# Kernel tuning notes

Measured on AMD Instinct MI355X. Metric: run time of the kernel, lower is better.

Reference implementation:

```python
import jax, jax.numpy as jnp
import numpy as np

RES = (256, 256, 256)

# 8 cube corners for trilinear splat/interp
_CORNERS = jnp.array([[i, j, k] for i in (0, 1) for j in (0, 1) for k in (0, 1)], dtype=jnp.int32)


def _corner_idx_weights(pts):
    # pts: (B,P,3) in [0,1). Returns periodic corner indices (B,P,8,3) and trilinear weights (B,P,8).
    resf = jnp.array(RES, dtype=pts.dtype)
    x = pts * resf
    ind0 = jnp.floor(x)
    frac = x - ind0  # (B,P,3)
    idx = (ind0.astype(jnp.int32)[:, :, None, :] + _CORNERS) % jnp.array(RES, dtype=jnp.int32)
    w = jnp.prod(jnp.where(_CORNERS == 1, frac[:, :, None, :], 1.0 - frac[:, :, None, :]), axis=-1)
    return idx, w


def point_rasterize(pts, vals):
    # Periodic trilinear scatter of vals (B,P,F) at pts (B,P,3) into grid (B,r0,r1,r2,F).
    B, P, _ = pts.shape
    F = vals.shape[-1]
    idx, w = _corner_idx_weights(pts)
    flat = (idx[..., 0] * RES[1] + idx[..., 1]) * RES[2] + idx[..., 2]  # (B,P,8)
    contrib = vals[:, :, None, :] * w[..., None]  # (B,P,8,F)
    Rtot = RES[0] * RES[1] * RES[2]
    grid = jax.vmap(lambda s, c: jax.ops.segment_sum(c, s, num_segments=Rtot))(
        flat.reshape(B, -1), contrib.reshape(B, -1, F))
    return grid.reshape(B, RES[0], RES[1], RES[2], F)


def grid_interp(grid, pts):
    # Periodic trilinear gather from grid (B,r0,r1,r2) at pts (B,P,3) -> (B,P).
    B = pts.shape[0]
    idx, w = _corner_idx_weights(pts)
    b = jnp.arange(B)[:, None, None]
    vals = grid[b, idx[..., 0], idx[..., 1], idx[..., 2]]  # (B,P,8)
    return jnp.sum(vals * w, axis=-1)


def _fftfreqs():
    # integer frequencies (d=1/res), rfft freqs on the last axis; shape (r0,r1,rf,3)
    fx = np.fft.fftfreq(RES[0], d=1.0 / RES[0])
    fy = np.fft.fftfreq(RES[1], d=1.0 / RES[1])
    fz = np.fft.rfftfreq(RES[2], d=1.0 / RES[2])
    om = np.stack(np.meshgrid(fx, fy, fz, indexing='ij'), axis=-1)
    return jnp.asarray(om, dtype=jnp.float32)


def dpsr_forward(V, N):
    ras = point_rasterize(V, N)                     # (B,r0,r1,r2,3) splatted normals
    Nhat = jnp.fft.rfftn(ras, axes=(1, 2, 3))       # (B,r0,r1,rf,3) complex spectrum
    omega = _fftfreqs() * jnp.float32(2.0 * np.pi)  # (r0,r1,rf,3)
    DivN = jnp.sum(-1j * omega * Nhat, axis=-1)     # freq-domain divergence
    Lap = -jnp.sum(omega ** 2, axis=-1)             # (r0,r1,rf) Laplacian symbol
    Phi = DivN / (Lap + 1e-6)
    Phi = Phi.at[:, 0, 0, 0].set(0.0)               # zero the DC term
    phi = jnp.fft.irfftn(Phi, s=RES, axes=(1, 2, 3)).astype(jnp.float32)  # (B,r0,r1,r2)
    # shift: subtract mean field value at the input points
    fv = grid_interp(phi, V)                        # (B,P)
    offset = jnp.mean(fv, axis=-1)
    phi = phi - offset[:, None, None, None]
    # scale: normalize by |phi| at the grid origin
    fv0 = phi[:, 0, 0, 0]
    phi = -phi / jnp.abs(fv0)[:, None, None, None] * 0.5
    return phi


def setup_inputs() -> dict:
    key = jax.random.key(0)
    kV, kN = jax.random.split(key)
    V = jax.random.uniform(kV, (1, 100000, 3), dtype=jnp.float32)  # coords in [0,1)
    N = jax.random.normal(kN, (1, 100000, 3), dtype=jnp.float32)   # point normals
    return {"V": V, "N": N}


def reference(V, N):
    return dpsr_forward(V, N)
```

## Files before the change

kernel.cpp:

```cpp
#include <hip/hip_runtime.h>
#include <math.h>

#define NRES 256
#define NZK  129
#define NLINE_XY (NRES * NRES)
#define STRX (NRES * NZK)
#define NSPEC (NRES * NRES * NZK)
#define TWO_PI 6.283185307179586f

__device__ __forceinline__ void dft16(float2* v, float sgn) {
    const float C16[8] = {1.f, 0.923879532511287f, 0.707106781186548f, 0.382683432365090f,
                          0.f, -0.382683432365090f, -0.707106781186548f, -0.923879532511287f};
    const float S16[8] = {0.f, 0.382683432365090f, 0.707106781186548f, 0.923879532511287f,
                          1.f, 0.923879532511287f, 0.707106781186548f, 0.382683432365090f};
    float2 t[16];
    float2* src = v;
    float2* dst = t;
#pragma unroll
    for (int s = 0; s < 4; ++s) {
        const int st = 1 << s;
#pragma unroll
        for (int bb = 0; bb < 8; ++bb) {
            const int q = bb & (st - 1);
            const int p = bb >> s;
            const int m = p << s;
            float2 a = src[q + st * p];
            float2 b = src[q + st * p + 8];
            float cw = C16[m], sw = sgn * S16[m];
            float ar = a.x - b.x, ai = a.y - b.y;
            dst[q + st * 2 * p]       = make_float2(a.x + b.x, a.y + b.y);
            dst[q + st * (2 * p + 1)] = make_float2(ar * cw - ai * sw, ar * sw + ai * cw);
        }
        float2* tmp = src; src = dst; dst = tmp;
    }
}

__device__ __forceinline__ void twiddle_store(float2* J, const float2* v, int tl, int tx, float sgn) {
    float s1, c1;
    __sincosf(sgn * (TWO_PI / 256.f) * (float)tx, &s1, &c1);
    float wr = 1.f, wi = 0.f;
#pragma unroll
    for (int c = 0; c < 16; ++c) {
        float2 a = v[c];
        J[(c * 16 + tx) * 16 + tl] = make_float2(a.x * wr - a.y * wi, a.x * wi + a.y * wr);
        float nwr = wr * c1 - wi * s1;
        wi = wr * s1 + wi * c1;
        wr = nwr;
    }
}

__device__ __forceinline__ void twiddle_store32(float2* J, const float2* v, int tl, int tx, float sgn) {
    float s1, c1;
    __sincosf(sgn * (TWO_PI / 256.f) * (float)tx, &s1, &c1);
    float wr = 1.f, wi = 0.f;
#pragma unroll
    for (int c = 0; c < 16; ++c) {
        float2 a = v[c];
        J[(c * 16 + tx) * 32 + tl] = make_float2(a.x * wr - a.y * wi, a.x * wi + a.y * wr);
        float nwr = wr * c1 - wi * s1;
        wi = wr * s1 + wi * c1;
        wr = nwr;
    }
}

__global__ void kraster(const float* __restrict__ pts, const float* __restrict__ vals,
                        float* __restrict__ R, int P, int c) {
    int p = blockIdx.x * blockDim.x + threadIdx.x;
    if (p >= P) return;
    float px = pts[p * 3 + 0] * (float)NRES;
    float py = pts[p * 3 + 1] * (float)NRES;
    float pz = pts[p * 3 + 2] * (float)NRES;
    float fx0 = floorf(px), fy0 = floorf(py), fz0 = floorf(pz);
    int ix = ((int)fx0) & 255, iy = ((int)fy0) & 255, iz = ((int)fz0) & 255;
    float tx = px - fx0, ty = py - fy0, tz = pz - fz0;
    float v = vals[p * 3 + c];
    int ix1 = (ix + 1) & 255, iy1 = (iy + 1) & 255, iz1 = (iz + 1) & 255;
    float wx0 = 1.f - tx, wy0 = 1.f - ty, wz0 = 1.f - tz;
    atomicAdd(&R[((ix  * NRES + iy ) * NRES) + iz ], v * wx0 * wy0 * wz0);
    atomicAdd(&R[((ix  * NRES + iy ) * NRES) + iz1], v * wx0 * wy0 * tz );
    atomicAdd(&R[((ix  * NRES + iy1) * NRES) + iz ], v * wx0 * ty  * wz0);
    atomicAdd(&R[((ix  * NRES + iy1) * NRES) + iz1], v * wx0 * ty  * tz );
    atomicAdd(&R[((ix1 * NRES + iy ) * NRES) + iz ], v * tx  * wy0 * wz0);
    atomicAdd(&R[((ix1 * NRES + iy ) * NRES) + iz1], v * tx  * wy0 * tz );
    atomicAdd(&R[((ix1 * NRES + iy1) * NRES) + iz ], v * tx  * ty  * wz0);
    atomicAdd(&R[((ix1 * NRES + iy1) * NRES) + iz1], v * tx  * ty  * tz );
}

__global__ __launch_bounds__(256) void kfft_z_r2c(float* __restrict__ R,
                                                  float2* __restrict__ S,
                                                  int mulz, int zeroR) {
    __shared__ float2 Jb[4096];
    const int tl = threadIdx.x & 15;
    const int tx = threadIdx.x >> 4;
    const size_t lb = (size_t)blockIdx.x * 16;

    float* Rf = (float*)Jb;
    float4* rg = (float4*)(R + lb * NRES);
#pragma unroll
    for (int k = 0; k < 4; ++k) {
        int q = threadIdx.x + k * 256;
        float4 f = rg[q];
        int i = q >> 6;
        int z = (q & 63) << 2;
        Rf[i * 257 + z + 0] = f.x;
        Rf[i * 257 + z + 1] = f.y;
        Rf[i * 257 + z + 2] = f.z;
        Rf[i * 257 + z + 3] = f.w;
    }
    if (zeroR) {
        float4 zz = make_float4(0.f, 0.f, 0.f, 0.f);
#pragma unroll
        for (int k = 0; k < 4; ++k) rg[threadIdx.x + k * 256] = zz;
    }
    __syncthreads();
    float2 v[16];
#pragma unroll
    for (int j = 0; j < 16; ++j)
        v[j] = make_float2(Rf[tl * 257 + tx + 16 * j], 0.f);
    __syncthreads();
    dft16(v, -1.f);
    twiddle_store(Jb, v, tl, tx, -1.f);
    __syncthreads();
    float2 u[16];
#pragma unroll
    for (int j2 = 0; j2 < 16; ++j2) u[j2] = Jb[(tx * 16 + j2) * 16 + tl];
    dft16(u, -1.f);
    __syncthreads();
    float2* XL = Jb;
#pragma unroll
    for (int d = 0; d < 16; ++d) {
        int k = tx + 16 * d;
        if (k <= 128) {
            float2 a = u[d];
            if (mulz) {
                float w = TWO_PI * (float)k;
                a = make_float2(w * a.y, -w * a.x);
            }
            XL[tl * 131 + k] = a;
        }
    }
    __syncthreads();
    float2* sg = S + lb * NZK;
#pragma unroll
    for (int j = 0; j < 9; ++j) {
        int q = threadIdx.x + j * 256;
        if (q < 16 * NZK) {
            int i = q / NZK;
            int k = q - i * NZK;
            sg[q] = XL[i * 131 + k];
        }
    }
}

__global__ __launch_bounds__(512) void kfft_y(float2* __restrict__ S, float sgn) {
    __shared__ float2 Jb[8192];
    const int tl = threadIdx.x & 31;
    const int tx = threadIdx.x >> 5;
    const int xpl = blockIdx.x / 5;
    const int g = blockIdx.x % 5;
    const int zk = g * 32 + tl;
    const bool valid = zk < NZK;
    const size_t base = (size_t)xpl * STRX + (valid ? zk : 128);

    float2 v[16];
#pragma unroll
    for (int j = 0; j < 16; ++j) {
        int y = tx + 16 * j;
        v[j] = valid ? S[base + (size_t)y * NZK] : make_float2(0.f, 0.f);
    }
    dft16(v, sgn);
    twiddle_store32(Jb, v, tl, tx, sgn);
    __syncthreads();
    float2 u[16];
#pragma unroll
    for (int j2 = 0; j2 < 16; ++j2) u[j2] = Jb[(tx * 16 + j2) * 32 + tl];
    dft16(u, sgn);
#pragma unroll
    for (int d = 0; d < 16; ++d) {
        int y = tx + 16 * d;
        if (valid) S[base + (size_t)y * NZK] = u[d];
    }
}

__global__ __launch_bounds__(512) void kfft_y2(float2* __restrict__ A,
                                               const float2* __restrict__ B) {
    __shared__ float2 Jb[8192];
    const int tl = threadIdx.x & 31;
    const int tx = threadIdx.x >> 5;
    const int xpl = blockIdx.x / 5;
    const int g = blockIdx.x % 5;
    const int zk = g * 32 + tl;
    const bool valid = zk < NZK;
    const size_t base = (size_t)xpl * STRX + (valid ? zk : 128);

    float2 vA[16], vB[16];
#pragma unroll
    for (int j = 0; j < 16; ++j) {
        size_t addr = base + (size_t)(tx + 16 * j) * NZK;
        vA[j] = valid ? A[addr] : make_float2(0.f, 0.f);
        vB[j] = valid ? B[addr] : make_float2(0.f, 0.f);
    }
    dft16(vA, -1.f);
    twiddle_store32(Jb, vA, tl, tx, -1.f);
    __syncthreads();
    float2 uA[16];
#pragma unroll
    for (int j2 = 0; j2 < 16; ++j2) uA[j2] = Jb[(tx * 16 + j2) * 32 + tl];
    dft16(uA, -1.f);
    __syncthreads();
    dft16(vB, -1.f);
    twiddle_store32(Jb, vB, tl, tx, -1.f);
    __syncthreads();
    float2 uB[16];
#pragma unroll
    for (int j2 = 0; j2 < 16; ++j2) uB[j2] = Jb[(tx * 16 + j2) * 32 + tl];
    dft16(uB, -1.f);
#pragma unroll
    for (int d = 0; d < 16; ++d) {
        int y = tx + 16 * d;
        float wy = TWO_PI * (float)(y < 128 ? y : y - 256);
        float2 a = uA[d], b = uB[d];
        a.x += wy * b.y;
        a.y -= wy * b.x;
        if (valid) A[base + (size_t)y * NZK] = a;
    }
}

__global__ __launch_bounds__(256) void kfft_x_mega(float2* __restrict__ A,
                                                   const float2* __restrict__ B) {
    __shared__ float2 Jb[4096];
    const int tl = threadIdx.x & 15;
    const int tx = threadIdx.x >> 4;
    const int l = blockIdx.x * 16 + tl;
    const int y = l / NZK;
    const int zk = l - y * NZK;
    const float fy = (float)(y < 128 ? y : y - 256);
    const float fz = (float)zk;
    const float w2 = TWO_PI * TWO_PI;
    const float invN3 = 1.0f / 16777216.0f;

    float2 vA[16], vB[16];
#pragma unroll
    for (int j = 0; j < 16; ++j) {
        size_t addr = (size_t)(tx + 16 * j) * STRX + l;
        vA[j] = A[addr];
        vB[j] = B[addr];
    }
    dft16(vA, -1.f);
    twiddle_store(Jb, vA, tl, tx, -1.f);
    __syncthreads();
    float2 uT[16];
#pragma unroll
    for (int j2 = 0; j2 < 16; ++j2) uT[j2] = Jb[(tx * 16 + j2) * 16 + tl];
    dft16(uT, -1.f);
    __syncthreads();
    dft16(vB, -1.f);
    twiddle_store(Jb, vB, tl, tx, -1.f);
    __syncthreads();
    float2 uX[16];
#pragma unroll
    for (int j2 = 0; j2 < 16; ++j2) uX[j2] = Jb[(tx * 16 + j2) * 16 + tl];
    dft16(uX, -1.f);
    __syncthreads();
    float2 s[16];
#pragma unroll
    for (int d = 0; d < 16; ++d) {
        int xk = tx + 16 * d;
        float fx = (float)(xk < 128 ? xk : xk - 256);
        float wx = TWO_PI * fx;
        float2 a = uT[d], b = uX[d];
        a.x += wx * b.y;
        a.y -= wx * b.x;
        float lap = -(fx * fx + fy * fy + fz * fz) * w2;
        float scale = (xk == 0 && l == 0) ? 0.0f : (invN3 / (lap + 1e-6f));
        s[d] = make_float2(a.x * scale, a.y * scale);
    }
    dft16(s, 1.f);
    twiddle_store(Jb, s, tl, tx, 1.f);
    __syncthreads();
    float2 u[16];
#pragma unroll
    for (int j2 = 0; j2 < 16; ++j2) u[j2] = Jb[(tx * 16 + j2) * 16 + tl];
    dft16(u, 1.f);
#pragma unroll
    for (int d = 0; d < 16; ++d)
        A[(size_t)(tx + 16 * d) * STRX + l] = u[d];
}

__global__ __launch_bounds__(256) void kfft_z_c2r(const float2* __restrict__ S,
                                                  float* __restrict__ out) {
    __shared__ float2 Jb[4096];
    const int tl = threadIdx.x & 15;
    const int tx = threadIdx.x >> 4;
    const size_t lb = (size_t)blockIdx.x * 16;

    float2* SL = Jb;
    const float2* sg = S + lb * NZK;
#pragma unroll
    for (int j = 0; j < 9; ++j) {
        int q = threadIdx.x + j * 256;
        if (q < 16 * NZK) {
            int i = q / NZK;
            int k = q - i * NZK;
            SL[i * 131 + k] = sg[q];
        }
    }
    __syncthreads();
    float2 v[16];
#pragma unroll
    for (int j = 0; j < 16; ++j) {
        int z = tx + 16 * j;
        if (z <= 128) {
            v[j] = SL[tl * 131 + z];
        } else {
            float2 a = SL[tl * 131 + (256 - z)];
            v[j] = make_float2(a.x, -a.y);
        }
    }
    __syncthreads();
    dft16(v, 1.f);
    twiddle_store(Jb, v, tl, tx, 1.f);
    __syncthreads();
    float2 u[16];
#pragma unroll
    for (int j2 = 0; j2 < 16; ++j2) u[j2] = Jb[(tx * 16 + j2) * 16 + tl];
    dft16(u, 1.f);
    __syncthreads();
    float* Xr = (float*)Jb;
#pragma unroll
    for (int d = 0; d < 16; ++d)
        Xr[tl * 257 + tx + 16 * d] = u[d].x;
    __syncthreads();
    float4* og = (float4*)(out + lb * NRES);
#pragma unroll
    for (int k = 0; k < 4; ++k) {
        int q = threadIdx.x + k * 256;
        int i = q >> 6;
        int z = (q & 63) << 2;
        og[q] = make_float4(Xr[i * 257 + z + 0], Xr[i * 257 + z + 1],
                            Xr[i * 257 + z + 2], Xr[i * 257 + z + 3]);
    }
}

__global__ void kinterp(const float* __restrict__ pts, const float* __restrict__ phi,
                        float* __restrict__ wsS, int P) {
    int p = blockIdx.x * blockDim.x + threadIdx.x;
    float fv = 0.0f;
    if (p < P) {
        float px = pts[p * 3 + 0] * (float)NRES;
        float py = pts[p * 3 + 1] * (float)NRES;
        float pz = pts[p * 3 + 2] * (float)NRES;
        float fx0 = floorf(px), fy0 = floorf(py), fz0 = floorf(pz);
        int ix = ((int)fx0) & 255, iy = ((int)fy0) & 255, iz = ((int)fz0) & 255;
        float tx = px - fx0, ty = py - fy0, tz = pz - fz0;
        int ix1 = (ix + 1) & 255, iy1 = (iy + 1) & 255, iz1 = (iz + 1) & 255;
        float wx0 = 1.f - tx, wy0 = 1.f - ty, wz0 = 1.f - tz;
        fv =  phi[((ix  * NRES + iy ) * NRES) + iz ] * wx0 * wy0 * wz0
            + phi[((ix  * NRES + iy ) * NRES) + iz1] * wx0 * wy0 * tz
            + phi[((ix  * NRES + iy1) * NRES) + iz ] * wx0 * ty  * wz0
            + phi[((ix  * NRES + iy1) * NRES) + iz1] * wx0 * ty  * tz
            + phi[((ix1 * NRES + iy ) * NRES) + iz ] * tx  * wy0 * wz0
            + phi[((ix1 * NRES + iy ) * NRES) + iz1] * tx  * wy0 * tz
            + phi[((ix1 * NRES + iy1) * NRES) + iz ] * tx  * ty  * wz0
            + phi[((ix1 * NRES + iy1) * NRES) + iz1] * tx  * ty  * tz;
    }
#pragma unroll
    for (int off = 32; off > 0; off >>= 1) fv += __shfl_down(fv, off);
    __shared__ float wsum[4];
    int lane = threadIdx.x & 63, wid = threadIdx.x >> 6;
    if (lane == 0) wsum[wid] = fv;
    __syncthreads();
    if (threadIdx.x == 0) {
        float t = 0.0f;
        for (int i = 0; i < (int)(blockDim.x >> 6); ++i) t += wsum[i];
        atomicAdd(&wsS[0], t);
    }
    if (blockIdx.x == 0 && threadIdx.x == 0) wsS[1] = phi[0];
}

__global__ void kfinal(float4* __restrict__ out, const float* __restrict__ wsS, float invP) {
    int idx = blockIdx.x * blockDim.x + threadIdx.x;
    float offset = wsS[0] * invP;
    float fv0 = wsS[1] - offset;
    float sc = -0.5f / fabsf(fv0);
    float4 o = out[idx];
    o.x = (o.x - offset) * sc;
    o.y = (o.y - offset) * sc;
    o.z = (o.z - offset) * sc;
    o.w = (o.w - offset) * sc;
    out[idx] = o;
}

extern "C" void kernel_launch(void* const* d_in, const int* in_sizes, int n_in,
                              void* d_out, int out_size, void* d_ws, size_t ws_size,
                              hipStream_t stream) {
    const float* V = (const float*)d_in[0];
    const float* N = (const float*)d_in[1];
    float* out = (float*)d_out;
    const int P = in_sizes[0] / 3;

    float2* A = (float2*)d_ws;
    float2* B = A + NSPEC;
    float*  R = (float*)(B + NSPEC);
    float*  wsS = R + (size_t)NRES * NRES * NRES;

    const int rasterBlocks = (P + 255) / 256;
    const int zBlocks = NLINE_XY / 16;
    const int yBlocks = NRES * 5;
    const int xBlocks = STRX / 16;

    hipMemsetAsync(R, 0, (size_t)NRES * NRES * NRES * sizeof(float), stream);
    kraster<<<rasterBlocks, 256, 0, stream>>>(V, N, R, P, 2);
    kfft_z_r2c<<<zBlocks, 256, 0, stream>>>(R, A, 1, 1);

    kraster<<<rasterBlocks, 256, 0, stream>>>(V, N, R, P, 1);
    kfft_z_r2c<<<zBlocks, 256, 0, stream>>>(R, B, 0, 1);

    kfft_y2<<<yBlocks, 512, 0, stream>>>(A, B);

    kraster<<<rasterBlocks, 256, 0, stream>>>(V, N, R, P, 0);
    kfft_z_r2c<<<zBlocks, 256, 0, stream>>>(R, B, 0, 0);
    kfft_y<<<yBlocks, 512, 0, stream>>>(B, -1.0f);

    kfft_x_mega<<<xBlocks, 256, 0, stream>>>(A, B);

    kfft_y<<<yBlocks, 512, 0, stream>>>(A, +1.0f);
    kfft_z_c2r<<<zBlocks, 256, 0, stream>>>(A, out);

    hipMemsetAsync(wsS, 0, 2 * sizeof(float), stream);
    kinterp<<<rasterBlocks, 256, 0, stream>>>(V, out, wsS, P);
    kfinal<<<NLINE_XY / 4, 256, 0, stream>>>((float4*)out, wsS, 1.0f / (float)P);
}
```

Baseline: 453.7 us.

## Sort points by xy cell before rasterization to localize atomic scatters

Adds a counting sort of the points by their (x,y) grid cell: a histogram, a single-block scan and a scatter into sorted point and value buffers. All three rasterization passes then read the sorted arrays, so atomics from neighbouring threads land on nearby grid addresses and get better cache locality with less scattered memory traffic. The extra kernels and launches add overhead, and the sort scratch is carved out of the output buffer, which is only written later by the inverse FFT.

After: 494.4 us. 1.09x slower.

```diff
diff --git a/kernel.cpp b/kernel.cpp
--- a/kernel.cpp
+++ b/kernel.cpp
@@ -7,6 +7,7 @@
 #define STRX (NRES * NZK)
 #define NSPEC (NRES * NRES * NZK)
 #define TWO_PI 6.283185307179586f
+#define NBIN 65536
 
 __device__ __forceinline__ void dft16(float2* v, float sgn) {
     const float C16[8] = {1.f, 0.923879532511287f, 0.707106781186548f, 0.382683432365090f,
@@ -61,6 +62,58 @@
         wi = wr * s1 + wi * c1;
         wr = nwr;
     }
+}
+
+__device__ __forceinline__ int cell_of(const float* __restrict__ pts, int p) {
+    float px = pts[p * 3 + 0] * (float)NRES;
+    float py = pts[p * 3 + 1] * (float)NRES;
+    int ix = ((int)floorf(px)) & 255;
+    int iy = ((int)floorf(py)) & 255;
+    return (ix << 8) | iy;
+}
+
+__global__ void khist(const float* __restrict__ pts, int* __restrict__ hist, int P) {
+    int p = blockIdx.x * blockDim.x + threadIdx.x;
+    if (p >= P) return;
+    atomicAdd(&hist[cell_of(pts, p)], 1);
+}
+
+__global__ __launch_bounds__(1024) void kscan(const int* __restrict__ hist,
+                                              int* __restrict__ offs) {
+    __shared__ int part[1024];
+    const int tid = threadIdx.x;
+    const int base = tid * 64;
+    int s = 0;
+#pragma unroll
+    for (int i = 0; i < 64; ++i) s += hist[base + i];
+    part[tid] = s;
+    __syncthreads();
+    for (int off = 1; off < 1024; off <<= 1) {
+        int v = (tid >= off) ? part[tid - off] : 0;
+        __syncthreads();
+        part[tid] += v;
+        __syncthreads();
+    }
+    int run = (tid > 0) ? part[tid - 1] : 0;
+#pragma unroll
+    for (int i = 0; i < 64; ++i) {
+        offs[base + i] = run;
+        run += hist[base + i];
+    }
+}
+
+__global__ void kscatter(const float* __restrict__ pts, const float* __restrict__ vals,
+                         int* __restrict__ offs, float* __restrict__ spts,
+                         float* __restrict__ svals, int P) {
+    int p = blockIdx.x * blockDim.x + threadIdx.x;
+    if (p >= P) return;
+    int idx = atomicAdd(&offs[cell_of(pts, p)], 1);
+    spts[idx * 3 + 0] = pts[p * 3 + 0];
+    spts[idx * 3 + 1] = pts[p * 3 + 1];
+    spts[idx * 3 + 2] = pts[p * 3 + 2];
+    svals[idx * 3 + 0] = vals[p * 3 + 0];
+    svals[idx * 3 + 1] = vals[p * 3 + 1];
+    svals[idx * 3 + 2] = vals[p * 3 + 2];
 }
 
 __global__ void kraster(const float* __restrict__ pts, const float* __restrict__ vals,
@@ -404,21 +457,31 @@
     float*  R = (float*)(B + NSPEC);
     float*  wsS = R + (size_t)NRES * NRES * NRES;
 
+    int*   hist  = (int*)out;
+    int*   offs  = hist + NBIN;
+    float* spts  = (float*)(offs + NBIN);
+    float* svals = spts + 3 * P;
+
     const int rasterBlocks = (P + 255) / 256;
     const int zBlocks = NLINE_XY / 16;
     const int yBlocks = NRES * 5;
     const int xBlocks = STRX / 16;
 
+    hipMemsetAsync(hist, 0, NBIN * sizeof(int), stream);
+    khist<<<rasterBlocks, 256, 0, stream>>>(V, hist, P);
+    kscan<<<1, 1024, 0, stream>>>(hist, offs);
+    kscatter<<<rasterBlocks, 256, 0, stream>>>(V, N, offs, spts, svals, P);
+
     hipMemsetAsync(R, 0, (size_t)NRES * NRES * NRES * sizeof(float), stream);
-    kraster<<<rasterBlocks, 256, 0, stream>>>(V, N, R, P, 2);
+    kraster<<<rasterBlocks, 256, 0, stream>>>(spts, svals, R, P, 2);
     kfft_z_r2c<<<zBlocks, 256, 0, stream>>>(R, A, 1, 1);
 
-    kraster<<<rasterBlocks, 256, 0, stream>>>(V, N, R, P, 1);
+    kraster<<<rasterBlocks, 256, 0, stream>>>(spts, svals, R, P, 1);
     kfft_z_r2c<<<zBlocks, 256, 0, stream>>>(R, B, 0, 1);
 
     kfft_y2<<<yBlocks, 512, 0, stream>>>(A, B);
 
-    kraster<<<rasterBlocks, 256, 0, stream>>>(V, N, R, P, 0);
+    kraster<<<rasterBlocks, 256, 0, stream>>>(spts, svals, R, P, 0);
     kfft_z_r2c<<<zBlocks, 256, 0, stream>>>(R, B, 0, 0);
     kfft_y<<<yBlocks, 512, 0, stream>>>(B, -1.0f);
 
```
